# Optimization experiments

Hardware: AMD Instinct MI355X
Metric: run time of the kernel (lower is better)

Reference implementation:

```python
import jax, jax.numpy as jnp
import numpy as np

B, S, D = 2, 4096, 512   # batch, seq_len, hidden_dim
H, E = 8, 64             # n_heads, head_dim


def setup_inputs() -> dict:
    key = jax.random.key(0)
    ks = jax.random.split(key, 14)
    s = 0.02  # init scale
    return {
        "x":  jax.random.normal(ks[0], (B, S, D), dtype=jnp.float32),
        # stacked per-head projection weights, stored as [H, in, out]
        "wq": jax.random.normal(ks[1], (H, D, E), dtype=jnp.float32) * s,
        "bq": jax.random.normal(ks[2], (H, E), dtype=jnp.float32) * s,
        "wk": jax.random.normal(ks[3], (H, D, E), dtype=jnp.float32) * s,
        "bk": jax.random.normal(ks[4], (H, E), dtype=jnp.float32) * s,
        "wv": jax.random.normal(ks[5], (H, D, E), dtype=jnp.float32) * s,
        "bv": jax.random.normal(ks[6], (H, E), dtype=jnp.float32) * s,
        "wo": jax.random.normal(ks[7], (H, E, D), dtype=jnp.float32) * s,
        "bo": jax.random.normal(ks[8], (H, D), dtype=jnp.float32) * s,
        # MLP: Linear(D,D) -> ReLU -> Linear(D,D), stored as [in, out]
        "w1": jax.random.normal(ks[9], (D, D), dtype=jnp.float32) * s,
        "b1": jax.random.normal(ks[10], (D,), dtype=jnp.float32) * s,
        "w2": jax.random.normal(ks[11], (D, D), dtype=jnp.float32) * s,
        "b2": jax.random.normal(ks[12], (D,), dtype=jnp.float32) * s,
    }


def reference(x, wq, bq, wk, bk, wv, bv, wo, bo, w1, b1, w2, b2):
    # Per-head projections, batched over heads: [B, H, S, E]
    q = jnp.einsum('bsd,hde->bhse', x, wq) + bq[None, :, None, :]
    k = jnp.einsum('bsd,hde->bhse', x, wk) + bk[None, :, None, :]
    v = jnp.einsum('bsd,hde->bhse', x, wv) + bv[None, :, None, :]
    scale = 1.0 / jnp.sqrt(jnp.asarray(q.shape[-1], q.dtype))
    scores = jnp.einsum('bhse,bhte->bhst', q, k) * scale  # [B,H,S,S]
    A = jax.nn.softmax(scores, axis=-1)
    ctx = jnp.einsum('bhst,bhte->bhse', A, v)             # [B,H,S,E]
    # w_o per head then sum over heads (each head adds its bias once)
    y = jnp.einsum('bhse,hed->bsd', ctx, wo) + jnp.sum(bo, axis=0)
    # MLP
    h = jax.nn.relu(y @ w1 + b1)
    return h @ w2 + b2
```

## Files before the change

### kernel.cpp

```cpp
#include <hip/hip_runtime.h>
#include <math.h>

#define Bsz 2
#define Sq  4096
#define Dm  512
#define Hn  8
#define Eh  64

typedef unsigned short u16;
typedef __attribute__((ext_vector_type(8))) short bf16x8;
typedef __attribute__((ext_vector_type(4))) short bf16x4;
typedef __attribute__((ext_vector_type(4))) float f32x4;
typedef __attribute__((ext_vector_type(4))) unsigned short u16x4;

#define KSCALE 0.18033688011112042f

__device__ __forceinline__ f32x4 mfma_16x16x16(bf16x4 a, bf16x4 b, f32x4 c) {
#if defined(__HIP_DEVICE_COMPILE__)
#if __has_builtin(__builtin_amdgcn_mfma_f32_16x16x16bf16_1k)
    return __builtin_amdgcn_mfma_f32_16x16x16bf16_1k(a, b, c, 0, 0, 0);
#else
    f32x4 d;
    asm volatile("v_mfma_f32_16x16x16_bf16 %0, %1, %2, %3"
                 : "=v"(d) : "v"(a), "v"(b), "v"(c));
    return d;
#endif
#else
    (void)a; (void)b;
    return c;
#endif
}

__device__ __forceinline__ u16 f2bf(float f) {
    unsigned int u = __float_as_uint(f);
    u += 0x7FFFu + ((u >> 16) & 1u);
    return (u16)(u >> 16);
}

__device__ __forceinline__ float fast_exp2(float x) {
#if defined(__HIP_DEVICE_COMPILE__) && __has_builtin(__builtin_amdgcn_exp2f)
    return __builtin_amdgcn_exp2f(x);
#else
    return exp2f(x);
#endif
}

__device__ __forceinline__ void async16(const u16* g, u16* l) {
    __builtin_amdgcn_global_load_lds(
        (const __attribute__((address_space(1))) void*)g,
        (__attribute__((address_space(3))) void*)l, 16, 0, 0);
}

template<int TN, int NT>
__device__ __forceinline__ void gemm_core(
    const u16* __restrict__ A, const u16* __restrict__ WT,
    int m0, int n0, u16* Ast, u16* Bst, f32x4 (&acc)[4][NT])
{
    const int tid  = threadIdx.x;
    const int lane = tid & 63, wid = tid >> 6;
    const int l15  = lane & 15, quad = lane >> 4;
    const int wm = wid >> 1, wn = wid & 1;

    for (int kt = 0; kt < Dm / 64; ++kt) {
        const int k0 = kt * 64;
        __syncthreads();
#pragma unroll
        for (int j = 0; j < 4; ++j) {
            int ci = wid * 256 + j * 64 + lane;
            int row = ci >> 3, c = (ci & 7) ^ (row & 7);
            async16(&A[(size_t)(m0 + row) * Dm + k0 + c * 8],
                    &Ast[(size_t)(wid * 256 + j * 64) * 8]);
        }
#pragma unroll
        for (int j = 0; j < TN / 32; ++j) {
            int ci = wid * (TN * 2) + j * 64 + lane;
            int row = ci >> 3, c = (ci & 7) ^ (row & 7);
            async16(&WT[(size_t)(n0 + row) * Dm + k0 + c * 8],
                    &Bst[(size_t)(wid * (TN * 2) + j * 64) * 8]);
        }
        __syncthreads();
#pragma unroll
        for (int ks = 0; ks < 2; ++ks) {
            bf16x8 af[4], bfr[NT];
#pragma unroll
            for (int mt = 0; mt < 4; ++mt) {
                int r = wm * 64 + mt * 16 + l15;
                af[mt] = *(const bf16x8*)&Ast[(r * 8 + ((ks * 4 + quad) ^ (r & 7))) * 8];
            }
#pragma unroll
            for (int nt = 0; nt < NT; ++nt) {
                int n = wn * (TN / 2) + nt * 16 + l15;
                bfr[nt] = *(const bf16x8*)&Bst[(n * 8 + ((ks * 4 + quad) ^ (n & 7))) * 8];
            }
#pragma unroll
            for (int mt = 0; mt < 4; ++mt)
#pragma unroll
                for (int nt = 0; nt < NT; ++nt)
                    acc[mt][nt] = __builtin_amdgcn_mfma_f32_16x16x32_bf16(
                        af[mt], bfr[nt], acc[mt][nt], 0, 0, 0);
        }
    }
}

__global__ __launch_bounds__(256) void prep_kernel(
    const float* __restrict__ x,
    const float* __restrict__ wq, const float* __restrict__ wk,
    const float* __restrict__ wv, const float* __restrict__ wo,
    const float* __restrict__ w1, const float* __restrict__ w2,
    const float* __restrict__ bo,
    u16* __restrict__ xb, u16* __restrict__ wqkvT, u16* __restrict__ woT,
    u16* __restrict__ w1T, u16* __restrict__ w2T, float* __restrict__ bo_s)
{
    const int seg = blockIdx.y, bx = blockIdx.x, tid = threadIdx.x;
    if (seg == 0) {
        const float4* xi = (const float4*)x;
        for (int i = bx * 256 + tid; i < (Bsz * Sq * Dm) / 4; i += 64 * 256) {
            float4 v = xi[i];
            u16x4 o = {f2bf(v.x), f2bf(v.y), f2bf(v.z), f2bf(v.w)};
            *(u16x4*)&xb[(size_t)i * 4] = o;
        }
        return;
    }
    if (seg == 7) {
        int d = bx * 256 + tid;
        if (d < Dm) {
            float s = 0.0f;
#pragma unroll
            for (int h = 0; h < Hn; ++h) s += bo[h * Dm + d];
            bo_s[d] = s;
        }
        return;
    }
    __shared__ float t[64][65];
    const float* src; u16* dst; int ld_in;
    if (seg <= 3) {
        const float* w = (seg == 1) ? wq : (seg == 2) ? wk : wv;
        int head = bx >> 3, kt = bx & 7;
        src = w + (size_t)head * Dm * Eh + (size_t)kt * 64 * 64;
        ld_in = 64;
        dst = wqkvT + ((size_t)((seg - 1) * 8 + head) * 64) * 512 + kt * 64;
    } else {
        const float* w = (seg == 4) ? wo : (seg == 5) ? w1 : w2;
        u16* dT = (seg == 4) ? woT : (seg == 5) ? w1T : w2T;
        int tr = bx >> 3, tc = bx & 7;
        src = w + (size_t)(tr * 64) * 512 + tc * 64;
        ld_in = 512;
        dst = dT + (size_t)(tc * 64) * 512 + tr * 64;
    }
#pragma unroll
    for (int it = 0; it < 16; ++it) {
        int idx = it * 256 + tid;
        int r = idx >> 6, c = idx & 63;
        t[r][c] = src[(size_t)r * ld_in + c];
    }
    __syncthreads();
#pragma unroll
    for (int it = 0; it < 4; ++it) {
        int idx = it * 256 + tid;
        int oc = idx >> 4, og = idx & 15;
        u16x4 o;
#pragma unroll
        for (int j = 0; j < 4; ++j) o[j] = f2bf(t[og * 4 + j][oc]);
        *(u16x4*)&dst[(size_t)oc * 512 + og * 4] = o;
    }
}

__global__ __launch_bounds__(256, 2) void qkv_gemm(
    const u16* __restrict__ xb, const u16* __restrict__ wqkvT,
    const float* __restrict__ bq, const float* __restrict__ bk,
    const float* __restrict__ bv,
    u16* __restrict__ qb, u16* __restrict__ kb, u16* __restrict__ vbT)
{
    __shared__ __align__(16) u16 Ast[128 * 64];
    __shared__ __align__(16) u16 Bst[64 * 64];
    const int proj = blockIdx.y >> 3, h = blockIdx.y & 7;
    const u16* WT = wqkvT + (size_t)blockIdx.y * 64 * 512;

    f32x4 acc[4][2];
#pragma unroll
    for (int i = 0; i < 4; ++i)
#pragma unroll
        for (int j = 0; j < 2; ++j) acc[i][j] = (f32x4)0.0f;

    gemm_core<64, 2>(xb, WT, blockIdx.x * 128, 0, Ast, Bst, acc);

    const int tid = threadIdx.x;
    const int lane = tid & 63, wid = tid >> 6;
    const int l15 = lane & 15, quad = lane >> 4;
    const int wm = wid >> 1, wn = wid & 1;
    const float* bias = (proj == 0) ? bq : (proj == 1) ? bk : bv;

    const int mbase = blockIdx.x * 128 + wm * 64;
    const int b = mbase >> 12;
    const int sbase = (mbase & (Sq - 1));
    const int bh = b * Hn + h;

#pragma unroll
    for (int mt = 0; mt < 4; ++mt)
#pragma unroll
        for (int nt = 0; nt < 2; ++nt) {
            int e = wn * 32 + nt * 16 + l15;
            float bval = bias[h * Eh + e];
            int s = sbase + mt * 16 + quad * 4;
            if (proj == 2) {
                u16x4 o;
#pragma unroll
                for (int r = 0; r < 4; ++r) o[r] = f2bf(acc[mt][nt][r] + bval);
                *(u16x4*)&vbT[((size_t)bh * Eh + e) * Sq + s] = o;
            } else if (proj == 1) {
                for (int r = 0; r < 4; ++r)
                    kb[((size_t)bh * Sq + s + r) * Eh + e] =
                        f2bf((acc[mt][nt][r] + bval) * KSCALE);
            } else {
                for (int r = 0; r < 4; ++r)
                    qb[((size_t)bh * Sq + s + r) * Eh + e] = f2bf(acc[mt][nt][r] + bval);
            }
        }
}

__global__ __launch_bounds__(256, 2) void attn_kernel(
    const u16* __restrict__ qb, const u16* __restrict__ kb,
    const u16* __restrict__ vbT, u16* __restrict__ ctxb)
{
    __shared__ __align__(16) u16 kst[2][64 * 64];
    __shared__ __align__(16) u16 vst[2][64 * 64];

    const int tid  = threadIdx.x;
    const int lane = tid & 63, wid = tid >> 6;
    const int l15  = lane & 15, quad = lane >> 4;
    const int bh = blockIdx.y;
    const int q0 = blockIdx.x * 128;
    const int b = bh >> 3, h = bh & 7;

    const u16* qg = qb + (size_t)bh * Sq * Eh;
    const u16* kg = kb + (size_t)bh * Sq * Eh;
    const u16* vg = vbT + (size_t)bh * Eh * Sq;

    int srow[2], scol[2];
#pragma unroll
    for (int j = 0; j < 2; ++j) {
        int ci = wid * 128 + j * 64 + lane;
        srow[j] = ci >> 3;
        scol[j] = (ci & 7) ^ (srow[j] & 7);
    }

    bf16x8 qf[2][2];
#pragma unroll
    for (int qt = 0; qt < 2; ++qt)
#pragma unroll
        for (int ks = 0; ks < 2; ++ks)
            qf[qt][ks] = *(const bf16x8*)&qg[(size_t)(q0 + wid * 32 + qt * 16 + l15) * Eh + ks * 32 + quad * 8];

    f32x4 O[4][2];
    float lp[2];
#pragma unroll
    for (int et = 0; et < 4; ++et)
#pragma unroll
        for (int qt = 0; qt < 2; ++qt) O[et][qt] = (f32x4)0.0f;
    lp[0] = lp[1] = 0.0f;

#pragma unroll
    for (int j = 0; j < 2; ++j) {
        async16(&kg[(size_t)srow[j] * Eh + scol[j] * 8],
                &kst[0][(wid * 128 + j * 64) * 8]);
        async16(&vg[(size_t)srow[j] * Sq + scol[j] * 8],
                &vst[0][(wid * 128 + j * 64) * 8]);
    }

    for (int kt = 0; kt < Sq / 64; ++kt) {
        const int cur = kt & 1;
        __syncthreads();

        if (kt < Sq / 64 - 1) {
            const int t1 = (kt + 1) * 64;
#pragma unroll
            for (int j = 0; j < 2; ++j) {
                async16(&kg[(size_t)(t1 + srow[j]) * Eh + scol[j] * 8],
                        &kst[cur ^ 1][(wid * 128 + j * 64) * 8]);
                async16(&vg[(size_t)srow[j] * Sq + t1 + scol[j] * 8],
                        &vst[cur ^ 1][(wid * 128 + j * 64) * 8]);
            }
        }

        const u16* kcur = kst[cur];
        const u16* vcur = vst[cur];

        f32x4 S[4][2];
#pragma unroll
        for (int tt = 0; tt < 4; ++tt)
#pragma unroll
            for (int qt = 0; qt < 2; ++qt) S[tt][qt] = (f32x4)0.0f;
#pragma unroll
        for (int ks = 0; ks < 2; ++ks)
#pragma unroll
            for (int tt = 0; tt < 4; ++tt) {
                int t = tt * 16 + l15;
                bf16x8 kf = *(const bf16x8*)&kcur[t * 64 + ((ks * 4 + quad) ^ (t & 7)) * 8];
                S[tt][0] = __builtin_amdgcn_mfma_f32_16x16x32_bf16(kf, qf[0][ks], S[tt][0], 0, 0, 0);
                S[tt][1] = __builtin_amdgcn_mfma_f32_16x16x32_bf16(kf, qf[1][ks], S[tt][1], 0, 0, 0);
            }

        bf16x4 pf[4][2];
#pragma unroll
        for (int tt = 0; tt < 4; ++tt)
#pragma unroll
            for (int qt = 0; qt < 2; ++qt)
#pragma unroll
                for (int r = 0; r < 4; ++r) {
                    float p = fast_exp2(S[tt][qt][r]);
                    lp[qt] += p;
                    pf[tt][qt][r] = (short)(__float_as_uint(p) >> 16);
                }

#pragma unroll
        for (int et = 0; et < 4; ++et) {
            int e = et * 16 + l15;
            bf16x4 vf[4];
#pragma unroll
            for (int tt = 0; tt < 4; ++tt) {
                int chunk = (tt * 2 + (quad >> 1)) ^ (e & 7);
                vf[tt] = *(const bf16x4*)&vcur[e * 64 + chunk * 8 + (quad & 1) * 4];
            }
#pragma unroll
            for (int qt = 0; qt < 2; ++qt)
#pragma unroll
                for (int tt = 0; tt < 4; ++tt)
                    O[et][qt] = mfma_16x16x16(vf[tt], pf[tt][qt], O[et][qt]);
        }
    }

#pragma unroll
    for (int qt = 0; qt < 2; ++qt) {
        float v = lp[qt];
        v += __shfl_xor(v, 16, 64);
        v += __shfl_xor(v, 32, 64);
        lp[qt] = v;
    }

#pragma unroll
    for (int qt = 0; qt < 2; ++qt) {
        const int qglob = q0 + wid * 32 + qt * 16 + l15;
        const float rl = 1.0f / lp[qt];
        u16* crow = ctxb + ((size_t)(b * Sq + qglob) * Hn + h) * Eh;
#pragma unroll
        for (int et = 0; et < 4; ++et) {
            u16x4 o;
#pragma unroll
            for (int r = 0; r < 4; ++r) o[r] = f2bf(O[et][qt][r] * rl);
            *(u16x4*)&crow[et * 16 + quad * 4] = o;
        }
    }
}

template<int MODE>
__global__ __launch_bounds__(256, 2) void gemmMN(
    const u16* __restrict__ A, const u16* __restrict__ WT,
    const float* __restrict__ bias, void* __restrict__ Cout)
{
    __shared__ __align__(16) u16 Ast[128 * 64];
    __shared__ __align__(16) u16 Bst[64 * 64];

    f32x4 acc[4][2];
#pragma unroll
    for (int i = 0; i < 4; ++i)
#pragma unroll
        for (int j = 0; j < 2; ++j) acc[i][j] = (f32x4)0.0f;

    gemm_core<64, 2>(A, WT, blockIdx.x * 128, blockIdx.y * 64, Ast, Bst, acc);

    const int tid = threadIdx.x;
    const int lane = tid & 63, wid = tid >> 6;
    const int l15 = lane & 15, quad = lane >> 4;
    const int m0 = blockIdx.x * 128 + (wid >> 1) * 64;
    const int n0 = blockIdx.y * 64 + (wid & 1) * 32;

#pragma unroll
    for (int mt = 0; mt < 4; ++mt)
#pragma unroll
        for (int nt = 0; nt < 2; ++nt) {
            int col = n0 + nt * 16 + l15;
            float bval = bias[col];
#pragma unroll
            for (int r = 0; r < 4; ++r) {
                int row = m0 + mt * 16 + quad * 4 + r;
                float v = acc[mt][nt][r] + bval;
                if (MODE == 1) v = fmaxf(v, 0.0f);
                if (MODE == 2) ((float*)Cout)[(size_t)row * Dm + col] = v;
                else           ((u16*)Cout)[(size_t)row * Dm + col] = f2bf(v);
            }
        }
}

extern "C" void kernel_launch(void* const* d_in, const int* in_sizes, int n_in,
                              void* d_out, int out_size, void* d_ws, size_t ws_size,
                              hipStream_t stream)
{
    const float* x  = (const float*)d_in[0];
    const float* wq = (const float*)d_in[1];
    const float* bq = (const float*)d_in[2];
    const float* wk = (const float*)d_in[3];
    const float* bk = (const float*)d_in[4];
    const float* wv = (const float*)d_in[5];
    const float* bv = (const float*)d_in[6];
    const float* wo = (const float*)d_in[7];
    const float* bo = (const float*)d_in[8];
    const float* w1 = (const float*)d_in[9];
    const float* b1 = (const float*)d_in[10];
    const float* w2 = (const float*)d_in[11];
    const float* b2 = (const float*)d_in[12];
    float* out = (float*)d_out;
    char* wsb = (char*)d_ws;

    const size_t MB = 1u << 20;
    u16*   xb    = (u16*)(wsb + 0);
    u16*   qb    = (u16*)(wsb + 8 * MB);
    u16*   kb    = (u16*)(wsb + 16 * MB);
    u16*   vbT   = (u16*)(wsb + 24 * MB);
    u16*   ctxb  = (u16*)(wsb + 32 * MB);
    u16*   ybuf  = (u16*)(wsb + 40 * MB);
    u16*   h1    = (u16*)(wsb + 48 * MB);
    u16*   wqkvT = (u16*)(wsb + 56 * MB);
    u16*   woT   = (u16*)(wsb + 58 * MB);
    u16*   w1T   = (u16*)(wsb + 59 * MB);
    u16*   w2T   = (u16*)(wsb + 60 * MB);
    float* bo_s  = (float*)(wsb + 61 * MB);

    prep_kernel<<<dim3(64, 8), 256, 0, stream>>>(
        x, wq, wk, wv, wo, w1, w2, bo, xb, wqkvT, woT, w1T, w2T, bo_s);
    qkv_gemm<<<dim3(Sq * Bsz / 128, 24), 256, 0, stream>>>(
        xb, wqkvT, bq, bk, bv, qb, kb, vbT);
    attn_kernel<<<dim3(Sq / 128, Bsz * Hn), 256, 0, stream>>>(qb, kb, vbT, ctxb);
    gemmMN<0><<<dim3(Bsz * Sq / 128, Dm / 64), 256, 0, stream>>>(ctxb, woT, bo_s, ybuf);
    gemmMN<1><<<dim3(Bsz * Sq / 128, Dm / 64), 256, 0, stream>>>(ybuf, w1T, b1, h1);
    gemmMN<2><<<dim3(Bsz * Sq / 128, Dm / 64), 256, 0, stream>>>(h1, w2T, b2, out);
}
```

Before: 251.7 us.

## Double-buffer the shared-memory tiles in the GEMM core

Result: slower. 257.0 us (+2.1%).

```diff
diff --git a/kernel.cpp b/kernel.cpp
--- a/kernel.cpp
+++ b/kernel.cpp
@@ -61,36 +61,61 @@
     const int l15  = lane & 15, quad = lane >> 4;
     const int wm = wid >> 1, wn = wid & 1;
 
+    int arow[4], acol[4];
+#pragma unroll
+    for (int j = 0; j < 4; ++j) {
+        int ci = wid * 256 + j * 64 + lane;
+        arow[j] = ci >> 3;
+        acol[j] = (ci & 7) ^ (arow[j] & 7);
+    }
+    int brow[TN / 32], bcol[TN / 32];
+#pragma unroll
+    for (int j = 0; j < TN / 32; ++j) {
+        int ci = wid * (TN * 2) + j * 64 + lane;
+        brow[j] = ci >> 3;
+        bcol[j] = (ci & 7) ^ (brow[j] & 7);
+    }
+
+#pragma unroll
+    for (int j = 0; j < 4; ++j)
+        async16(&A[(size_t)(m0 + arow[j]) * Dm + acol[j] * 8],
+                &Ast[(wid * 256 + j * 64) * 8]);
+#pragma unroll
+    for (int j = 0; j < TN / 32; ++j)
+        async16(&WT[(size_t)(n0 + brow[j]) * Dm + bcol[j] * 8],
+                &Bst[(wid * (TN * 2) + j * 64) * 8]);
+
     for (int kt = 0; kt < Dm / 64; ++kt) {
-        const int k0 = kt * 64;
+        const int cur = kt & 1;
         __syncthreads();
-#pragma unroll
-        for (int j = 0; j < 4; ++j) {
-            int ci = wid * 256 + j * 64 + lane;
-            int row = ci >> 3, c = (ci & 7) ^ (row & 7);
-            async16(&A[(size_t)(m0 + row) * Dm + k0 + c * 8],
-                    &Ast[(size_t)(wid * 256 + j * 64) * 8]);
-        }
-#pragma unroll
-        for (int j = 0; j < TN / 32; ++j) {
-            int ci = wid * (TN * 2) + j * 64 + lane;
-            int row = ci >> 3, c = (ci & 7) ^ (row & 7);
-            async16(&WT[(size_t)(n0 + row) * Dm + k0 + c * 8],
-                    &Bst[(size_t)(wid * (TN * 2) + j * 64) * 8]);
-        }
-        __syncthreads();
+
+        if (kt + 1 < Dm / 64) {
+            const int k1 = (kt + 1) * 64;
+            const int nx = cur ^ 1;
+#pragma unroll
+            for (int j = 0; j < 4; ++j)
+                async16(&A[(size_t)(m0 + arow[j]) * Dm + k1 + acol[j] * 8],
+                        &Ast[nx * 128 * 64 + (wid * 256 + j * 64) * 8]);
+#pragma unroll
+            for (int j = 0; j < TN / 32; ++j)
+                async16(&WT[(size_t)(n0 + brow[j]) * Dm + k1 + bcol[j] * 8],
+                        &Bst[nx * TN * 64 + (wid * (TN * 2) + j * 64) * 8]);
+        }
+
+        const u16* Acur = Ast + cur * 128 * 64;
+        const u16* Bcur = Bst + cur * TN * 64;
 #pragma unroll
         for (int ks = 0; ks < 2; ++ks) {
             bf16x8 af[4], bfr[NT];
 #pragma unroll
             for (int mt = 0; mt < 4; ++mt) {
                 int r = wm * 64 + mt * 16 + l15;
-                af[mt] = *(const bf16x8*)&Ast[(r * 8 + ((ks * 4 + quad) ^ (r & 7))) * 8];
+                af[mt] = *(const bf16x8*)&Acur[(r * 8 + ((ks * 4 + quad) ^ (r & 7))) * 8];
             }
 #pragma unroll
             for (int nt = 0; nt < NT; ++nt) {
                 int n = wn * (TN / 2) + nt * 16 + l15;
-                bfr[nt] = *(const bf16x8*)&Bst[(n * 8 + ((ks * 4 + quad) ^ (n & 7))) * 8];
+                bfr[nt] = *(const bf16x8*)&Bcur[(n * 8 + ((ks * 4 + quad) ^ (n & 7))) * 8];
             }
 #pragma unroll
             for (int mt = 0; mt < 4; ++mt)
@@ -171,8 +196,8 @@
     const float* __restrict__ bv,
     u16* __restrict__ qb, u16* __restrict__ kb, u16* __restrict__ vbT)
 {
-    __shared__ __align__(16) u16 Ast[128 * 64];
-    __shared__ __align__(16) u16 Bst[64 * 64];
+    __shared__ __align__(16) u16 Ast[2 * 128 * 64];
+    __shared__ __align__(16) u16 Bst[2 * 64 * 64];
     const int proj = blockIdx.y >> 3, h = blockIdx.y & 7;
     const u16* WT = wqkvT + (size_t)blockIdx.y * 64 * 512;
 
@@ -357,8 +382,8 @@
     const u16* __restrict__ A, const u16* __restrict__ WT,
     const float* __restrict__ bias, void* __restrict__ Cout)
 {
-    __shared__ __align__(16) u16 Ast[128 * 64];
-    __shared__ __align__(16) u16 Bst[64 * 64];
+    __shared__ __align__(16) u16 Ast[2 * 128 * 64];
+    __shared__ __align__(16) u16 Bst[2 * 64 * 64];
 
     f32x4 acc[4][2];
 #pragma unroll
```
